# Kernel tuning notes

Measured on AMD Instinct MI355X. Metric: run time of the kernel, lower is better.

The kernel has to match this reference:

```python
import jax, jax.numpy as jnp
import numpy as np

GRID_N = 256          # hardcoded 256x256 grid in the module
D = 64                # conv channel width
NL = 18               # module applications used (9 conv + 9 PReLU, interleaved)
LABEL_NC = 19
STYLE_DIM = 512


def setup_inputs() -> dict:
    key = jax.random.key(0)
    ks = jax.random.split(key, 7)
    B, C = 2, LABEL_NC
    x = jax.random.randint(ks[0], (B, C, GRID_N, GRID_N), 0, 2).astype(jnp.int32)
    conv_w0 = jax.random.normal(ks[1], (D, 2), dtype=jnp.float32) * 0.1
    conv_w = jax.random.normal(ks[2], (8, D, D), dtype=jnp.float32) * 0.05
    conv_b = jax.random.normal(ks[3], (9, D), dtype=jnp.float32) * 0.01
    prelu_a = jnp.full((9, D), 0.25, dtype=jnp.float32)  # PReLU default init
    fc_w = jax.random.normal(ks[4], (NL, STYLE_DIM, D * C), dtype=jnp.float32)
    fc_b = jnp.zeros((NL, STYLE_DIM), dtype=jnp.float32)
    return dict(x=x, conv_w0=conv_w0, conv_w=conv_w, conv_b=conv_b,
                prelu_a=prelu_a, fc_w=fc_w, fc_b=fc_b)


def _point_features(pts, conv_w0, conv_w, conv_b, prelu_a):
    """pts: (P,2). Returns (NL, P, D): snapshot after each of the 18 modules
    (conv, prelu, conv, prelu, ...) -- exactly what the original max-pools."""
    snaps = []
    z = pts @ conv_w0.T + conv_b[0]            # Conv1d(2,64,1) == pointwise linear
    snaps.append(z)
    z = jnp.where(z > 0, z, prelu_a[0] * z)    # PReLU(64)
    snaps.append(z)
    for i in range(8):
        z = z @ conv_w[i].T + conv_b[i + 1]
        snaps.append(z)
        z = jnp.where(z > 0, z, prelu_a[i + 1] * z)
        snaps.append(z)
    return jnp.stack(snaps)                    # (18, P, D)


def reference(x, conv_w0, conv_w, conv_b, prelu_a, fc_w, fc_b):
    B, C = x.shape[0], x.shape[1]
    P = GRID_N * GRID_N
    lin = jnp.linspace(-1.0, 1.0, GRID_N, dtype=jnp.float32)
    gx, gy = jnp.meshgrid(lin, lin)            # numpy default 'xy' indexing
    pts = jnp.stack([gx.reshape(-1), gy.reshape(-1)], axis=-1)   # (P, 2)

    # Grid points are shared by every (b, c): compute features once.
    snaps = _point_features(pts, conv_w0, conv_w, conv_b, prelu_a)        # (18, P, D)
    zero_snaps = _point_features(jnp.zeros((1, 2), jnp.float32),
                                 conv_w0, conv_w, conv_b, prelu_a)[:, 0]  # (18, D)

    mask = (x.reshape(B, C, P) == 1)           # (B, C, P)
    empty = ~jnp.any(mask, axis=-1)            # (B, C): original falls back to a zero point

    neg = jnp.float32(-jnp.inf)
    pooled = []
    for l in range(NL):                        # fixed, small layer loop
        pl = jnp.max(jnp.where(mask[..., None], snaps[l][None, None], neg), axis=2)  # (B,C,D)
        pl = jnp.where(empty[..., None], zero_snaps[l][None, None], pl)
        pooled.append(pl)
    pooled = jnp.stack(pooled, axis=1)         # (B, 18, C, D)
    feat = pooled.reshape(B, NL, C * D)        # channel-major concat, matches torch.cat dim=2

    # EqualLinear: out = x @ (W * scale).T + bias, scale = 1/sqrt(in_dim), lr_mul=1
    scale = 1.0 / jnp.sqrt(jnp.float32(C * D))
    # fcs are applied in reversed layer order and concatenated in that order
    w_rev = fc_w[::-1] * scale                 # (18, 512, C*D)
    b_rev = fc_b[::-1]                         # (18, 512)
    out = jnp.einsum('bld,lsd->bls', feat[:, ::-1], w_rev) + b_rev[None]
    return out                                  # (B, 18, 512)
```

## Files before the change

### kernel.cpp

```cpp
#include <hip/hip_runtime.h>
#include <hip/hip_fp16.h>

#define NSET 38
#define NSNAP 9
#define PART (NSNAP*NSET*64)
#define PPB 64
#define HSTR 72
#define PSTR 72
#define WHALF (8*64*64)

typedef unsigned int uint;
typedef __fp16 half8 __attribute__((ext_vector_type(8)));
typedef float  f32x4 __attribute__((ext_vector_type(4)));

#define HNEGINF 0xFC00u

static __device__ __forceinline__ uint pk_add(uint a, uint b) {
  uint r;
  asm("v_pk_add_f16 %0, %1, %2" : "=v"(r) : "v"(a), "v"(b));
  return r;
}
static __device__ __forceinline__ uint pk_max(uint a, uint b) {
  uint r;
  asm("v_pk_max_f16 %0, %1, %2" : "=v"(r) : "v"(a), "v"(b));
  return r;
}
static __device__ __forceinline__ float half_lo_f(uint u) {
  return (float)__builtin_bit_cast(__fp16, (unsigned short)(u & 0xFFFFu));
}
static __device__ __forceinline__ float half_hi_f(uint u) {
  return (float)__builtin_bit_cast(__fp16, (unsigned short)(u >> 16));
}

template<int CHUNKS>
__global__ __launch_bounds__(256)
void kA(const int* __restrict__ x, const float* __restrict__ w0,
        const float* __restrict__ cw, const float* __restrict__ cb,
        const float* __restrict__ pa, const __fp16* __restrict__ wf,
        float* __restrict__ partial)
{
  __shared__ __fp16 zth[PPB * HSTR];
  __shared__ __fp16 ztp[64 * PSTR];
  __shared__ uint   addp[40 * 32];
  __shared__ uint   memb2[PPB * 2];
  __shared__ float  padl[1024];

  const int tid = threadIdx.x;
  const int q  = tid & 63;
  const int g  = __builtin_amdgcn_readfirstlane(tid >> 6);
  const int l  = tid & 63;
  const int lr = l & 15;
  const int lg = l >> 4;
  const int sbase = g * 10;
  const int nset = (g == 3) ? 8 : 10;

  if ((int)blockIdx.x < 0) padl[tid] = 0.f;

  #pragma unroll 1
  for (int c = 0; c < CHUNKS; ++c) {
    const int p = (blockIdx.x * CHUNKS + c) * PPB + q;

    if (c) __syncthreads();
    if (tid < 128) {
      const int half = tid >> 6;
      uint m = 0;
      #pragma unroll
      for (int j = 0; j < 19; ++j)
        m |= (uint)(x[(half * 19 + j) * 65536 + p] == 1) << j;
      memb2[q * 2 + half] = m;
    }
    __syncthreads();

    #pragma unroll
    for (int i = tid; i < 1280; i += 256) {
      int j = i >> 5, pr = i & 31;
      uint lo0 = memb2[(2 * pr) * 2],     hi0 = memb2[(2 * pr) * 2 + 1];
      uint lo1 = memb2[(2 * pr + 1) * 2], hi1 = memb2[(2 * pr + 1) * 2 + 1];
      uint b0 = (j < 19) ? ((lo0 >> j) & 1u) : (j < 38) ? ((hi0 >> (j - 19)) & 1u) : 0u;
      uint b1 = (j < 19) ? ((lo1 >> j) & 1u) : (j < 38) ? ((hi1 >> (j - 19)) & 1u) : 0u;
      addp[i] = (b0 ? 0u : HNEGINF) | ((b1 ? 0u : HNEGINF) << 16);
    }

    float acc0[16];
    {
      float px = -1.f + (2.f / 255.f) * (float)(p & 255);
      float py = -1.f + (2.f / 255.f) * (float)(p >> 8);
      #pragma unroll
      for (int d = 0; d < 16; ++d) {
        int dd = (g << 4) + d;
        acc0[d] = fmaf(px, w0[2 * dd], fmaf(py, w0[2 * dd + 1], cb[dd]));
      }
    }
    __syncthreads();

    f32x4 Cf[4];

    #pragma unroll 1
    for (int s = 0; s < NSNAP; ++s) {
      if (s) __syncthreads();
      if (s == 0) {
        #pragma unroll
        for (int d = 0; d < 16; ++d) {
          int dd = (g << 4) + d;
          float zv = acc0[d];
          float a = pa[dd];
          float zp = zv > 0.f ? zv : a * zv;
          zth[q * HSTR + dd] = (__fp16)zp;
          ztp[dd * PSTR + q] = (__fp16)zp;
        }
      } else {
        #pragma unroll
        for (int dt = 0; dt < 4; ++dt) {
          int dim = (dt << 4) + lr;
          float a = pa[(s << 6) + dim];
          __fp16 zp[4];
          #pragma unroll
          for (int r = 0; r < 4; ++r) {
            float zv = Cf[dt][r];
            zp[r] = (__fp16)(zv > 0.f ? zv : a * zv);
            zth[((g << 4) + (lg << 2) + r) * HSTR + dim] = zp[r];
          }
          int pt0 = (g << 4) + (lg << 2);
          uint2 w2;
          w2.x = (uint)__builtin_bit_cast(unsigned short, zp[0]) |
                 ((uint)__builtin_bit_cast(unsigned short, zp[1]) << 16);
          w2.y = (uint)__builtin_bit_cast(unsigned short, zp[2]) |
                 ((uint)__builtin_bit_cast(unsigned short, zp[3]) << 16);
          *(uint2*)&ztp[dim * PSTR + pt0] = w2;
        }
      }
      __syncthreads();

      if (s < 8) {
        half8 a0 = *(const half8*)&zth[((g << 4) + lr) * HSTR + (lg << 3)];
        half8 a1 = *(const half8*)&zth[((g << 4) + lr) * HSTR + 32 + (lg << 3)];
        const __fp16* wb = wf + ((size_t)s << 12);
        #pragma unroll
        for (int dt = 0; dt < 4; ++dt) {
          float bias = cb[((s + 1) << 6) + (dt << 4) + lr];
          f32x4 a4 = {bias, bias, bias, bias};
          half8 b0 = *(const half8*)&wb[(((dt << 4) + lr) << 6) + (lg << 3)];
          half8 b1 = *(const half8*)&wb[(((dt << 4) + lr) << 6) + 32 + (lg << 3)];
          a4 = __builtin_amdgcn_mfma_f32_16x16x32_f16(a0, b0, a4, 0, 0, 0);
          a4 = __builtin_amdgcn_mfma_f32_16x16x32_f16(a1, b1, a4, 0, 0, 0);
          Cf[dt] = a4;
        }
      }

      uint run2[10];
      #pragma unroll
      for (int j = 0; j < 10; ++j) run2[j] = HNEGINF | (HNEGINF << 16);
      #pragma unroll 2
      for (int c4 = 0; c4 < 8; ++c4) {
        uint4 v4 = *(const uint4*)&ztp[q * PSTR + (c4 << 3)];
        #pragma unroll
        for (int j = 0; j < 10; ++j) {
          uint4 aj = *(const uint4*)&addp[((sbase + j) << 5) + (c4 << 2)];
          run2[j] = pk_max(run2[j], pk_add(v4.x, aj.x));
          run2[j] = pk_max(run2[j], pk_add(v4.y, aj.y));
          run2[j] = pk_max(run2[j], pk_add(v4.z, aj.z));
          run2[j] = pk_max(run2[j], pk_add(v4.w, aj.w));
        }
      }
      {
        float* pb = partial + (size_t)blockIdx.x * PART + s * (NSET * 64) + q;
        #pragma unroll
        for (int j = 0; j < 10; ++j) {
          if (j < nset) {
            float mx = fmaxf(half_lo_f(run2[j]), half_hi_f(run2[j]));
            int set = sbase + j;
            if (CHUNKS == 1 || c == 0) pb[set * 64] = mx;
            else                       pb[set * 64] = fmaxf(pb[set * 64], mx);
          }
        }
      }
    }
  }
}

__global__ __launch_bounds__(256) void kW(const float* __restrict__ cw,
                                          __fp16* __restrict__ wf)
{
  int i = blockIdx.x * 256 + threadIdx.x;
  if (i < WHALF) wf[i] = (__fp16)cw[i];
}

__global__ __launch_bounds__(256) void kB1(float* __restrict__ partial, int per)
{
  int idx = blockIdx.x * 256 + threadIdx.x;
  if (idx >= PART) return;
  float* p0 = partial + (size_t)blockIdx.y * per * PART + idx;
  float mx = -3e38f;
  #pragma unroll 8
  for (int b = 0; b < per; ++b)
    mx = fmaxf(mx, p0[(size_t)b * PART]);
  p0[0] = mx;
}

__global__ __launch_bounds__(256) void kB2(const float* __restrict__ partial,
    int per, const float* __restrict__ cw, const float* __restrict__ cb,
    const float* __restrict__ pa, float* __restrict__ feat)
{
  __shared__ float zl[64];
  __shared__ float zc[NSNAP][64];
  __shared__ float zp[NSNAP][64];
  int tid = threadIdx.x;
  int d = tid & 63;
  float z = cb[d];
  #pragma unroll 1
  for (int s = 0; s < NSNAP; ++s) {
    if (tid < 64) {
      zc[s][d] = z;
      float a = pa[(s << 6) + d];
      float v = z > 0.f ? z : a * z;
      zp[s][d] = v;
      zl[d] = v;
    }
    __syncthreads();
    if (s < 8) {
      if (tid < 64) {
        float a2 = cb[((s + 1) << 6) + d];
        for (int k = 0; k < 64; ++k)
          a2 = fmaf(zl[k], cw[(s << 12) + (d << 6) + k], a2);
        z = a2;
      }
    }
    __syncthreads();
  }

  int idx = blockIdx.x * 256 + tid;
  if (idx >= PART) return;
  int s = idx / (NSET * 64);
  int r = idx - s * (NSET * 64);
  int set = r >> 6;
  int dd = r & 63;
  float mx = -3e38f;
  #pragma unroll
  for (int y = 0; y < 32; ++y)
    mx = fmaxf(mx, partial[(size_t)y * per * PART + idx]);
  int b = set / 19, cc = set - b * 19;
  float even_v, odd_v;
  if (mx < -5e37f) {
    even_v = zc[s][dd];
    odd_v  = zp[s][dd];
  } else {
    odd_v = mx;
    float a = pa[(s << 6) + dd];
    even_v = mx > 0.f ? mx : mx / a;
  }
  size_t fb = ((size_t)b * 18 + 2 * s) * 1216 + cc * 64 + dd;
  feat[fb] = even_v;
  feat[fb + 1216] = odd_v;
}

__global__ __launch_bounds__(256) void kC(const float* __restrict__ feat,
    const float* __restrict__ fcw, const float* __restrict__ fcb,
    float* __restrict__ out)
{
  __shared__ float f0[1216], f1[1216];
  int lr = blockIdx.y;
  int chunk = blockIdx.x;
  int tid = threadIdx.x;
  for (int i = tid; i < 1216; i += 256) {
    f0[i] = feat[(size_t)(0 * 18 + lr) * 1216 + i];
    f1[i] = feat[(size_t)(1 * 18 + lr) * 1216 + i];
  }
  __syncthreads();
  int wv = tid >> 6, lane = tid & 63;
  float scale = 1.f / sqrtf(1216.f);
  int l = 17 - lr;
  #pragma unroll 1
  for (int rr = 0; rr < 4; ++rr) {
    int srow = (chunk << 4) + (wv << 2) + rr;
    const float* wrow = fcw + ((size_t)lr * 512 + srow) * 1216;
    float pp0 = 0.f, pp1 = 0.f;
    #pragma unroll
    for (int k = 0; k < 19; ++k) {
      float w = wrow[(k << 6) + lane];
      pp0 = fmaf(w, f0[(k << 6) + lane], pp0);
      pp1 = fmaf(w, f1[(k << 6) + lane], pp1);
    }
    #pragma unroll
    for (int off = 32; off; off >>= 1) {
      pp0 += __shfl_xor(pp0, off, 64);
      pp1 += __shfl_xor(pp1, off, 64);
    }
    if (lane == 0) {
      float b = fcb[lr * 512 + srow];
      out[((size_t)0 * 18 + l) * 512 + srow] = fmaf(scale, pp0, b);
      out[((size_t)1 * 18 + l) * 512 + srow] = fmaf(scale, pp1, b);
    }
  }
}

extern "C" void kernel_launch(void* const* d_in, const int* in_sizes, int n_in,
                              void* d_out, int out_size, void* d_ws, size_t ws_size,
                              hipStream_t stream) {
  const int*   x   = (const int*)d_in[0];
  const float* w0  = (const float*)d_in[1];
  const float* cw  = (const float*)d_in[2];
  const float* cb  = (const float*)d_in[3];
  const float* pa  = (const float*)d_in[4];
  const float* fcw = (const float*)d_in[5];
  const float* fcb = (const float*)d_in[6];
  float* ws = (float*)d_ws;
  float* out = (float*)d_out;

  const size_t tail = (size_t)2 * 18 * 1216 + WHALF / 2;
  #define NEED(n) (((size_t)(n) * PART + tail) * 4)

  int nblk;
  if      (ws_size >= NEED(1024)) nblk = 1024;
  else if (ws_size >= NEED(512))  nblk = 512;
  else                            nblk = 256;

  float* partial = ws;
  float* feat = ws + (size_t)nblk * PART;
  __fp16* wf = (__fp16*)(feat + (size_t)2 * 18 * 1216);
  const int per = nblk >> 5;

  hipLaunchKernelGGL(kW, dim3(WHALF / 256), dim3(256), 0, stream, cw, wf);

  if (nblk == 1024) {
    hipLaunchKernelGGL(kA<1>, dim3(1024), dim3(256), 0, stream,
                       x, w0, cw, cb, pa, wf, partial);
  } else if (nblk == 512) {
    hipLaunchKernelGGL(kA<2>, dim3(512), dim3(256), 0, stream,
                       x, w0, cw, cb, pa, wf, partial);
  } else {
    hipLaunchKernelGGL(kA<4>, dim3(256), dim3(256), 0, stream,
                       x, w0, cw, cb, pa, wf, partial);
  }

  hipLaunchKernelGGL(kB1, dim3(86, 32), dim3(256), 0, stream, partial, per);
  hipLaunchKernelGGL(kB2, dim3(86), dim3(256), 0, stream,
                     partial, per, cw, cb, pa, feat);
  hipLaunchKernelGGL(kC, dim3(32, 18), dim3(256), 0, stream, feat, fcw, fcb, out);
}
```

Before: 130.6 us.

## Process snapshot layers in pairs with double-buffered tiles and fp16 partials

```diff
diff --git a/kernel.cpp b/kernel.cpp
--- a/kernel.cpp
+++ b/kernel.cpp
@@ -10,51 +10,90 @@
 #define WHALF (8*64*64)
 
 typedef unsigned int uint;
-typedef __fp16 half8 __attribute__((ext_vector_type(8)));
+typedef __fp16 h2 __attribute__((ext_vector_type(2)));
+typedef __fp16 h4 __attribute__((ext_vector_type(4)));
+typedef __fp16 h8 __attribute__((ext_vector_type(8)));
 typedef float  f32x4 __attribute__((ext_vector_type(4)));
 
 #define HNEGINF 0xFC00u
 
-static __device__ __forceinline__ uint pk_add(uint a, uint b) {
-  uint r;
-  asm("v_pk_add_f16 %0, %1, %2" : "=v"(r) : "v"(a), "v"(b));
-  return r;
-}
-static __device__ __forceinline__ uint pk_max(uint a, uint b) {
-  uint r;
-  asm("v_pk_max_f16 %0, %1, %2" : "=v"(r) : "v"(a), "v"(b));
-  return r;
-}
-static __device__ __forceinline__ float half_lo_f(uint u) {
-  return (float)__builtin_bit_cast(__fp16, (unsigned short)(u & 0xFFFFu));
-}
-static __device__ __forceinline__ float half_hi_f(uint u) {
-  return (float)__builtin_bit_cast(__fp16, (unsigned short)(u >> 16));
-}
+static __device__ __forceinline__ h2 h2max(h2 a, h2 b) {
+  return __builtin_elementwise_max(a, b);
+}
+#define SPLIT8(v, v0, v1, v2, v3)                       \
+  h2 v0 = __builtin_shufflevector(v, v, 0, 1);          \
+  h2 v1 = __builtin_shufflevector(v, v, 2, 3);          \
+  h2 v2 = __builtin_shufflevector(v, v, 4, 5);          \
+  h2 v3 = __builtin_shufflevector(v, v, 6, 7);
 
 template<int CHUNKS>
 __global__ __launch_bounds__(256)
 void kA(const int* __restrict__ x, const float* __restrict__ w0,
         const float* __restrict__ cw, const float* __restrict__ cb,
         const float* __restrict__ pa, const __fp16* __restrict__ wf,
-        float* __restrict__ partial)
-{
-  __shared__ __fp16 zth[PPB * HSTR];
-  __shared__ __fp16 ztp[64 * PSTR];
-  __shared__ uint   addp[40 * 32];
-  __shared__ uint   memb2[PPB * 2];
-  __shared__ float  padl[1024];
+        __fp16* __restrict__ partialh)
+{
+  __shared__ __align__(16) __fp16 zth[PPB * HSTR];
+  __shared__ __align__(16) __fp16 ztpA[64 * PSTR];
+  __shared__ __align__(16) __fp16 ztpB[64 * PSTR];
+  __shared__ __align__(16) __fp16 addp[40 * 64];
+  __shared__ uint memb2[PPB * 2];
 
   const int tid = threadIdx.x;
   const int q  = tid & 63;
   const int g  = __builtin_amdgcn_readfirstlane(tid >> 6);
-  const int l  = tid & 63;
-  const int lr = l & 15;
-  const int lg = l >> 4;
+  const int lr = tid & 15;
+  const int lg = (tid & 63) >> 4;
   const int sbase = g * 10;
   const int nset = (g == 3) ? 8 : 10;
-
-  if ((int)blockIdx.x < 0) padl[tid] = 0.f;
+  const __fp16 HNI = __builtin_bit_cast(__fp16, (unsigned short)0xFC00);
+  const h2 H2NI = {HNI, HNI};
+
+  auto prelu_frag = [&](int sv, f32x4* C, __fp16* ztpX) {
+    #pragma unroll
+    for (int dt = 0; dt < 4; ++dt) {
+      int dim = (dt << 4) + lr;
+      float a = pa[(sv << 6) + dim];
+      __fp16 zp[4];
+      #pragma unroll
+      for (int r = 0; r < 4; ++r) {
+        float zv = C[dt][r];
+        zp[r] = (__fp16)(zv > 0.f ? zv : a * zv);
+        zth[((g << 4) + (lg << 2) + r) * HSTR + dim] = zp[r];
+      }
+      int pt0 = (g << 4) + (lg << 2);
+      h4 w4 = {zp[0], zp[1], zp[2], zp[3]};
+      *(h4*)&ztpX[dim * PSTR + pt0] = w4;
+    }
+  };
+  auto mfma_layer = [&](int sv, f32x4* C) {
+    h8 a0 = *(const h8*)&zth[((g << 4) + lr) * HSTR + (lg << 3)];
+    h8 a1 = *(const h8*)&zth[((g << 4) + lr) * HSTR + 32 + (lg << 3)];
+    const __fp16* wb = wf + ((size_t)sv << 12);
+    #pragma unroll
+    for (int dt = 0; dt < 4; ++dt) {
+      float bias = cb[((sv + 1) << 6) + (dt << 4) + lr];
+      f32x4 a4 = {bias, bias, bias, bias};
+      h8 b0 = *(const h8*)&wb[(((dt << 4) + lr) << 6) + (lg << 3)];
+      h8 b1 = *(const h8*)&wb[(((dt << 4) + lr) << 6) + 32 + (lg << 3)];
+      a4 = __builtin_amdgcn_mfma_f32_16x16x32_f16(a0, b0, a4, 0, 0, 0);
+      a4 = __builtin_amdgcn_mfma_f32_16x16x32_f16(a1, b1, a4, 0, 0, 0);
+      C[dt] = a4;
+    }
+  };
+  auto fold_store = [&](int sv, h2* runv, int c) {
+    __fp16* pb = partialh + (size_t)blockIdx.x * PART + sv * (NSET * 64) + q;
+    #pragma unroll
+    for (int j = 0; j < 10; ++j) {
+      if (j < nset) {
+        h2 r = runv[j];
+        __fp16 m = r.x > r.y ? r.x : r.y;
+        int off = (sbase + j) * 64;
+        if (CHUNKS == 1 || c == 0) pb[off] = m;
+        else { __fp16 o = pb[off]; pb[off] = (m > o) ? m : o; }
+      }
+    }
+  };
 
   #pragma unroll 1
   for (int c = 0; c < CHUNKS; ++c) {
@@ -71,14 +110,17 @@
     }
     __syncthreads();
 
-    #pragma unroll
-    for (int i = tid; i < 1280; i += 256) {
-      int j = i >> 5, pr = i & 31;
-      uint lo0 = memb2[(2 * pr) * 2],     hi0 = memb2[(2 * pr) * 2 + 1];
-      uint lo1 = memb2[(2 * pr + 1) * 2], hi1 = memb2[(2 * pr + 1) * 2 + 1];
-      uint b0 = (j < 19) ? ((lo0 >> j) & 1u) : (j < 38) ? ((hi0 >> (j - 19)) & 1u) : 0u;
-      uint b1 = (j < 19) ? ((lo1 >> j) & 1u) : (j < 38) ? ((hi1 >> (j - 19)) & 1u) : 0u;
-      addp[i] = (b0 ? 0u : HNEGINF) | ((b1 ? 0u : HNEGINF) << 16);
+    {
+      uint* addp32 = (uint*)addp;
+      #pragma unroll
+      for (int i = tid; i < 1280; i += 256) {
+        int j = i >> 5, pr = i & 31;
+        uint lo0 = memb2[(2 * pr) * 2],     hi0 = memb2[(2 * pr) * 2 + 1];
+        uint lo1 = memb2[(2 * pr + 1) * 2], hi1 = memb2[(2 * pr + 1) * 2 + 1];
+        uint b0 = (j < 19) ? ((lo0 >> j) & 1u) : (j < 38) ? ((hi0 >> (j - 19)) & 1u) : 0u;
+        uint b1 = (j < 19) ? ((lo1 >> j) & 1u) : (j < 38) ? ((hi1 >> (j - 19)) & 1u) : 0u;
+        addp32[i] = (b0 ? 0u : HNEGINF) | ((b1 ? 0u : HNEGINF) << 16);
+      }
     }
 
     float acc0[16];
@@ -93,87 +135,70 @@
     }
     __syncthreads();
 
-    f32x4 Cf[4];
-
-    #pragma unroll 1
-    for (int s = 0; s < NSNAP; ++s) {
-      if (s) __syncthreads();
-      if (s == 0) {
-        #pragma unroll
-        for (int d = 0; d < 16; ++d) {
-          int dd = (g << 4) + d;
-          float zv = acc0[d];
-          float a = pa[dd];
-          float zp = zv > 0.f ? zv : a * zv;
-          zth[q * HSTR + dd] = (__fp16)zp;
-          ztp[dd * PSTR + q] = (__fp16)zp;
-        }
-      } else {
-        #pragma unroll
-        for (int dt = 0; dt < 4; ++dt) {
-          int dim = (dt << 4) + lr;
-          float a = pa[(s << 6) + dim];
-          __fp16 zp[4];
-          #pragma unroll
-          for (int r = 0; r < 4; ++r) {
-            float zv = Cf[dt][r];
-            zp[r] = (__fp16)(zv > 0.f ? zv : a * zv);
-            zth[((g << 4) + (lg << 2) + r) * HSTR + dim] = zp[r];
-          }
-          int pt0 = (g << 4) + (lg << 2);
-          uint2 w2;
-          w2.x = (uint)__builtin_bit_cast(unsigned short, zp[0]) |
-                 ((uint)__builtin_bit_cast(unsigned short, zp[1]) << 16);
-          w2.y = (uint)__builtin_bit_cast(unsigned short, zp[2]) |
-                 ((uint)__builtin_bit_cast(unsigned short, zp[3]) << 16);
-          *(uint2*)&ztp[dim * PSTR + pt0] = w2;
-        }
-      }
-      __syncthreads();
-
-      if (s < 8) {
-        half8 a0 = *(const half8*)&zth[((g << 4) + lr) * HSTR + (lg << 3)];
-        half8 a1 = *(const half8*)&zth[((g << 4) + lr) * HSTR + 32 + (lg << 3)];
-        const __fp16* wb = wf + ((size_t)s << 12);
-        #pragma unroll
-        for (int dt = 0; dt < 4; ++dt) {
-          float bias = cb[((s + 1) << 6) + (dt << 4) + lr];
-          f32x4 a4 = {bias, bias, bias, bias};
-          half8 b0 = *(const half8*)&wb[(((dt << 4) + lr) << 6) + (lg << 3)];
-          half8 b1 = *(const half8*)&wb[(((dt << 4) + lr) << 6) + 32 + (lg << 3)];
-          a4 = __builtin_amdgcn_mfma_f32_16x16x32_f16(a0, b0, a4, 0, 0, 0);
-          a4 = __builtin_amdgcn_mfma_f32_16x16x32_f16(a1, b1, a4, 0, 0, 0);
-          Cf[dt] = a4;
-        }
-      }
-
-      uint run2[10];
-      #pragma unroll
-      for (int j = 0; j < 10; ++j) run2[j] = HNEGINF | (HNEGINF << 16);
+    #pragma unroll
+    for (int d = 0; d < 16; ++d) {
+      int dd = (g << 4) + d;
+      float zv = acc0[d];
+      float a = pa[dd];
+      __fp16 zp = (__fp16)(zv > 0.f ? zv : a * zv);
+      zth[q * HSTR + dd] = zp;
+      ztpA[dd * PSTR + q] = zp;
+    }
+    __syncthreads();
+
+    f32x4 Cf[4], Cf2[4];
+    mfma_layer(0, Cf);
+
+    {
+      h2 runA[10];
+      #pragma unroll
+      for (int j = 0; j < 10; ++j) runA[j] = H2NI;
       #pragma unroll 2
       for (int c4 = 0; c4 < 8; ++c4) {
-        uint4 v4 = *(const uint4*)&ztp[q * PSTR + (c4 << 3)];
+        h8 va = *(const h8*)&ztpA[q * PSTR + (c4 << 3)];
+        SPLIT8(va, va0, va1, va2, va3)
         #pragma unroll
         for (int j = 0; j < 10; ++j) {
-          uint4 aj = *(const uint4*)&addp[((sbase + j) << 5) + (c4 << 2)];
-          run2[j] = pk_max(run2[j], pk_add(v4.x, aj.x));
-          run2[j] = pk_max(run2[j], pk_add(v4.y, aj.y));
-          run2[j] = pk_max(run2[j], pk_add(v4.z, aj.z));
-          run2[j] = pk_max(run2[j], pk_add(v4.w, aj.w));
+          h8 a8 = *(const h8*)&addp[((sbase + j) << 6) + (c4 << 3)];
+          SPLIT8(a8, a0, a1, a2, a3)
+          runA[j] = h2max(runA[j],
+                     h2max(h2max(va0 + a0, va1 + a1), h2max(va2 + a2, va3 + a3)));
         }
       }
-      {
-        float* pb = partial + (size_t)blockIdx.x * PART + s * (NSET * 64) + q;
+      fold_store(0, runA, c);
+    }
+
+    #pragma unroll 1
+    for (int sp = 0; sp < 4; ++sp) {
+      const int s = 1 + 2 * sp;
+      __syncthreads();
+      prelu_frag(s, Cf, ztpA);
+      mfma_layer(s, Cf2);
+      prelu_frag(s + 1, Cf2, ztpB);
+      if (sp < 3) mfma_layer(s + 1, Cf);
+      __syncthreads();
+
+      h2 runA[10], runB[10];
+      #pragma unroll
+      for (int j = 0; j < 10; ++j) { runA[j] = H2NI; runB[j] = H2NI; }
+      #pragma unroll 2
+      for (int c4 = 0; c4 < 8; ++c4) {
+        h8 va = *(const h8*)&ztpA[q * PSTR + (c4 << 3)];
+        h8 vb = *(const h8*)&ztpB[q * PSTR + (c4 << 3)];
+        SPLIT8(va, va0, va1, va2, va3)
+        SPLIT8(vb, vb0, vb1, vb2, vb3)
         #pragma unroll
         for (int j = 0; j < 10; ++j) {
-          if (j < nset) {
-            float mx = fmaxf(half_lo_f(run2[j]), half_hi_f(run2[j]));
-            int set = sbase + j;
-            if (CHUNKS == 1 || c == 0) pb[set * 64] = mx;
-            else                       pb[set * 64] = fmaxf(pb[set * 64], mx);
-          }
+          h8 a8 = *(const h8*)&addp[((sbase + j) << 6) + (c4 << 3)];
+          SPLIT8(a8, a0, a1, a2, a3)
+          runA[j] = h2max(runA[j],
+                     h2max(h2max(va0 + a0, va1 + a1), h2max(va2 + a2, va3 + a3)));
+          runB[j] = h2max(runB[j],
+                     h2max(h2max(vb0 + a0, vb1 + a1), h2max(vb2 + a2, vb3 + a3)));
         }
       }
+      fold_store(s, runA, c);
+      fold_store(s + 1, runB, c);
     }
   }
 }
@@ -185,20 +210,21 @@
   if (i < WHALF) wf[i] = (__fp16)cw[i];
 }
 
-__global__ __launch_bounds__(256) void kB1(float* __restrict__ partial, int per)
+__global__ __launch_bounds__(256) void kB1(const __fp16* __restrict__ ph,
+    float* __restrict__ buf32, int per)
 {
   int idx = blockIdx.x * 256 + threadIdx.x;
   if (idx >= PART) return;
-  float* p0 = partial + (size_t)blockIdx.y * per * PART + idx;
+  const __fp16* p0 = ph + (size_t)blockIdx.y * per * PART + idx;
   float mx = -3e38f;
   #pragma unroll 8
   for (int b = 0; b < per; ++b)
-    mx = fmaxf(mx, p0[(size_t)b * PART]);
-  p0[0] = mx;
-}
-
-__global__ __launch_bounds__(256) void kB2(const float* __restrict__ partial,
-    int per, const float* __restrict__ cw, const float* __restrict__ cb,
+    mx = fmaxf(mx, (float)p0[(size_t)b * PART]);
+  buf32[(size_t)blockIdx.y * PART + idx] = mx;
+}
+
+__global__ __launch_bounds__(256) void kB2(const float* __restrict__ buf32,
+    const float* __restrict__ cw, const float* __restrict__ cb,
     const float* __restrict__ pa, float* __restrict__ feat)
 {
   __shared__ float zl[64];
@@ -237,7 +263,7 @@
   float mx = -3e38f;
   #pragma unroll
   for (int y = 0; y < 32; ++y)
-    mx = fmaxf(mx, partial[(size_t)y * per * PART + idx]);
+    mx = fmaxf(mx, buf32[(size_t)y * PART + idx]);
   int b = set / 19, cc = set - b * 19;
   float even_v, odd_v;
   if (mx < -5e37f) {
@@ -303,37 +329,39 @@
   const float* pa  = (const float*)d_in[4];
   const float* fcw = (const float*)d_in[5];
   const float* fcb = (const float*)d_in[6];
-  float* ws = (float*)d_ws;
   float* out = (float*)d_out;
-
-  const size_t tail = (size_t)2 * 18 * 1216 + WHALF / 2;
-  #define NEED(n) (((size_t)(n) * PART + tail) * 4)
+  char* base = (char*)d_ws;
+
+  #define NEED(n) ((size_t)(n) * PART * 2 + (size_t)32 * PART * 4 \
+                   + (size_t)2 * 18 * 1216 * 4 + (size_t)WHALF * 2)
 
   int nblk;
   if      (ws_size >= NEED(1024)) nblk = 1024;
   else if (ws_size >= NEED(512))  nblk = 512;
   else                            nblk = 256;
 
-  float* partial = ws;
-  float* feat = ws + (size_t)nblk * PART;
-  __fp16* wf = (__fp16*)(feat + (size_t)2 * 18 * 1216);
+  __fp16* partialh = (__fp16*)base;
+  float*  buf32 = (float*)(base + (size_t)nblk * PART * 2);
+  float*  feat  = buf32 + (size_t)32 * PART;
+  __fp16* wf    = (__fp16*)(feat + (size_t)2 * 18 * 1216);
   const int per = nblk >> 5;
 
   hipLaunchKernelGGL(kW, dim3(WHALF / 256), dim3(256), 0, stream, cw, wf);
 
   if (nblk == 1024) {
     hipLaunchKernelGGL(kA<1>, dim3(1024), dim3(256), 0, stream,
-                       x, w0, cw, cb, pa, wf, partial);
+                       x, w0, cw, cb, pa, wf, partialh);
   } else if (nblk == 512) {
     hipLaunchKernelGGL(kA<2>, dim3(512), dim3(256), 0, stream,
-                       x, w0, cw, cb, pa, wf, partial);
+                       x, w0, cw, cb, pa, wf, partialh);
   } else {
     hipLaunchKernelGGL(kA<4>, dim3(256), dim3(256), 0, stream,
-                       x, w0, cw, cb, pa, wf, partial);
-  }
-
-  hipLaunchKernelGGL(kB1, dim3(86, 32), dim3(256), 0, stream, partial, per);
+                       x, w0, cw, cb, pa, wf, partialh);
+  }
+
+  hipLaunchKernelGGL(kB1, dim3(86, 32), dim3(256), 0, stream,
+                     partialh, buf32, per);
   hipLaunchKernelGGL(kB2, dim3(86), dim3(256), 0, stream,
-                     partial, per, cw, cb, pa, feat);
+                     buf32, cw, cb, pa, feat);
   hipLaunchKernelGGL(kC, dim3(32, 18), dim3(256), 0, stream, feat, fcw, fcb, out);
 }
```

After: 133.3 us. 1.02x slower.
